# Kernel tuning notes

Measured on AMD Instinct MI355X. Metric: run time of the kernel, lower is better.

## Reference

```python
import jax, jax.numpy as jnp
import numpy as np


def setup_inputs() -> dict:
    key = jax.random.key(0)
    k1, k2, k3, k4 = jax.random.split(key, 4)
    T, B, D, S = 4096, 16, 128, 256
    inputs = jax.random.normal(k1, (T, B, D), dtype=jnp.float32)
    z0 = jnp.zeros((B, S), dtype=jnp.float32)
    # parameters, initialized as in the torch module
    log_neg_a = jnp.full((S,), -0.5, dtype=jnp.float32)
    b = jax.random.normal(k2, (S, D), dtype=jnp.float32) * 0.01
    log_dt = jnp.log(jnp.full((S,), 0.05, dtype=jnp.float32))
    return {"inputs": inputs, "z0": z0, "log_neg_a": log_neg_a, "b": b, "log_dt": log_dt}


def reference(inputs, z0, log_neg_a, b, log_dt):
    # discretized diagonal SSM parameters
    a_real = -jnp.exp(jnp.clip(log_neg_a, -8.0, 4.0))            # [S]
    dt = jnp.exp(jnp.clip(log_dt, -8.0, 1.0))                    # [S]
    a_bar = jnp.exp(dt * a_real)                                 # [S]
    x = dt * a_real
    ratio = jnp.where(jnp.abs(x) < 1e-6, dt, jnp.expm1(x) / a_real)
    b_bar = ratio[:, None] * b                                   # [S, D]

    # precompute input projection for all timesteps: [T, B, S]
    ub = jnp.einsum('tbd,sd->tbs', inputs, b_bar)

    def step(z, u_t):
        z = a_bar[None, :] * z + u_t                             # [B, S]
        return z, z

    _, outs = jax.lax.scan(step, z0, ub)                          # [T, B, S]
    return outs
```

## Files before the change

kernel.cpp:

```cpp
#include <hip/hip_runtime.h>
#include <hip/hip_bf16.h>

#define T_  4096
#define B_  16
#define D_  128
#define S_  256
#define WND 64
#define C4  (T_/WND)

using bf8   = __attribute__((ext_vector_type(8))) short;
using f32x4 = __attribute__((ext_vector_type(4))) float;

__device__ inline float bfbits(unsigned short h) {
    return __builtin_bit_cast(float, (unsigned)h << 16);
}
__device__ inline unsigned short bf16bits(float f) {
    return __hip_bfloat16_raw(__float2bfloat16(f)).x;
}

__global__ __launch_bounds__(256) void k_params(
        const float* __restrict__ lna, const float* __restrict__ bmat,
        const float* __restrict__ ldt,
        float* __restrict__ abar, float* __restrict__ a64,
        __hip_bfloat16* __restrict__ bbar) {
    if (blockIdx.x < 128) {
        int idx = blockIdx.x * 256 + threadIdx.x;
        int s = idx >> 7;
        float la = fminf(fmaxf(lna[s], -8.f), 4.f);
        float ar = -expf(la);
        float lt = fminf(fmaxf(ldt[s], -8.f), 1.f);
        float dt = expf(lt);
        float xx = dt * ar;
        float ratio = (fabsf(xx) < 1e-6f) ? dt : (expm1f(xx) / ar);
        bbar[idx] = __float2bfloat16(ratio * bmat[idx]);
    } else {
        int s = threadIdx.x;
        float la = fminf(fmaxf(lna[s], -8.f), 4.f);
        float ar = -expf(la);
        float lt = fminf(fmaxf(ldt[s], -8.f), 1.f);
        float dt = expf(lt);
        float ab = expf(dt * ar);
        abar[s] = ab;
        float p = ab;
#pragma unroll
        for (int j = 0; j < 6; ++j) p *= p;
        a64[s] = p;
    }
}

__global__ __launch_bounds__(256, 4) void k_gemm(
        const float* __restrict__ x, const __hip_bfloat16* __restrict__ bbar,
        const float* __restrict__ abar,
        __hip_bfloat16* __restrict__ ub, float* __restrict__ e64) {
    const int c = blockIdx.x, b = blockIdx.y;
    __shared__ char LDS[WND * 512];
    const int tid = threadIdx.x, lane = tid & 63, w = tid >> 6;
    const int l15 = lane & 15, l4 = lane >> 4;

    bf8 bfrag[4][4];
#pragma unroll
    for (int j = 0; j < 4; ++j) {
        int s = w * 64 + j * 16 + l15;
#pragma unroll
        for (int kk = 0; kk < 4; ++kk)
            bfrag[j][kk] = *(const bf8*)((const short*)bbar + s * D_ + kk * 32 + l4 * 8);
    }

#pragma unroll
    for (int k = 0; k < 8; ++k) {
        int idx = tid + k * 256;
        int row = idx >> 5, seg = idx & 31;
        float4 v = *(const float4*)(x + ((size_t)(c * WND + row) * B_ + b) * D_ + seg * 4);
        __hip_bfloat162 lo = __float22bfloat162_rn(make_float2(v.x, v.y));
        __hip_bfloat162 hi = __float22bfloat162_rn(make_float2(v.z, v.w));
        uint2 pk = { *(unsigned*)&lo, *(unsigned*)&hi };
        int off = (row * 256 + seg * 8) ^ ((row & 7) << 4);
        *(uint2*)(LDS + off) = pk;
    }
    __syncthreads();

    f32x4 acc[4][4] = {};
#pragma unroll
    for (int i = 0; i < 4; ++i) {
        bf8 af[4];
        int tr = i * 16 + l15;
#pragma unroll
        for (int kk = 0; kk < 4; ++kk) {
            int off = (tr * 256 + kk * 64 + l4 * 16) ^ ((tr & 7) << 4);
            af[kk] = *(const bf8*)(LDS + off);
        }
#pragma unroll
        for (int j = 0; j < 4; ++j)
#pragma unroll
            for (int kk = 0; kk < 4; ++kk)
                acc[i][j] = __builtin_amdgcn_mfma_f32_16x16x32_bf16(
                                af[kk], bfrag[j][kk], acc[i][j], 0, 0, 0);
    }
    __syncthreads();

#pragma unroll
    for (int j = 0; j < 4; ++j) {
        int s = w * 64 + j * 16 + l15;
        float a  = abar[s];
        float a2 = a * a, a4 = a2 * a2, a8 = a4 * a4, a16 = a8 * a8;
        float lf = (l4 == 0) ? a8 * a4 : (l4 == 1) ? a8 : (l4 == 2) ? a4 : 1.f;
        float e = 0.f;
#pragma unroll
        for (int i = 0; i < 4; ++i) {
            unsigned short h0 = bf16bits(acc[i][j][0]);
            unsigned short h1 = bf16bits(acc[i][j][1]);
            unsigned short h2 = bf16bits(acc[i][j][2]);
            unsigned short h3 = bf16bits(acc[i][j][3]);
            float inner = bfbits(h0);
            inner = fmaf(inner, a, bfbits(h1));
            inner = fmaf(inner, a, bfbits(h2));
            inner = fmaf(inner, a, bfbits(h3));
            e = fmaf(e, a16, inner);
            int row0 = i * 16 + l4 * 4;
            *(unsigned short*)(LDS + (((row0    ) * 512 + s * 2) ^ (l4 << 5))) = h0;
            *(unsigned short*)(LDS + (((row0 + 1) * 512 + s * 2) ^ (l4 << 5))) = h1;
            *(unsigned short*)(LDS + (((row0 + 2) * 512 + s * 2) ^ (l4 << 5))) = h2;
            *(unsigned short*)(LDS + (((row0 + 3) * 512 + s * 2) ^ (l4 << 5))) = h3;
        }
        e *= lf;
        e += __shfl_xor(e, 16);
        e += __shfl_xor(e, 32);
        if (l4 == 0) e64[((size_t)c * B_ + b) * S_ + s] = e;
    }
    __syncthreads();

    char* op = (char*)(ub + ((size_t)b * T_ + c * WND) * S_);
#pragma unroll
    for (int k = 0; k < 8; ++k) {
        int o = k * 4096 + tid * 16;
        int swz = (2 * k + (w >> 1)) & 3;
        uint4 v = *(uint4*)(LDS + (o ^ (swz << 5)));
        *(uint4*)(op + o) = v;
    }
}

__global__ __launch_bounds__(256) void k_scan(
        const __hip_bfloat16* __restrict__ ub, const float* __restrict__ e64,
        const float* __restrict__ abar, const float* __restrict__ a64,
        const float* __restrict__ z0, float* __restrict__ out) {
    const int c = blockIdx.x, g = blockIdx.y;
    const int w = threadIdx.x >> 6, lane = threadIdx.x & 63;
    const int b = g * 2 + (w >> 1);
    const int s0 = (w & 1) * 128 + lane * 2;

    float2 a  = *(const float2*)(abar + s0);
    float2 aw = *(const float2*)(a64 + s0);
    float2 z  = *(const float2*)(z0 + b * S_ + s0);

#pragma unroll
    for (int cp0 = 0; cp0 < C4; cp0 += 16) {
        float2 ev[16];
#pragma unroll
        for (int k = 0; k < 16; ++k)
            ev[k] = *(const float2*)(e64 + ((size_t)(cp0 + k) * B_ + b) * S_ + s0);
#pragma unroll
        for (int k = 0; k < 16; ++k) {
            float zx = fmaf(aw.x, z.x, ev[k].x);
            float zy = fmaf(aw.y, z.y, ev[k].y);
            bool p = (cp0 + k) < c;
            z.x = p ? zx : z.x;
            z.y = p ? zy : z.y;
        }
    }

    const char* up = (const char*)(ub + ((size_t)b * T_ + c * WND) * S_ + s0);
    float* op = out + ((size_t)(c * WND) * B_ + b) * S_ + s0;
#pragma unroll 8
    for (int t = 0; t < WND; ++t) {
        ushort2 v = *(const ushort2*)up;
        z.x = fmaf(a.x, z.x, bfbits(v.x));
        z.y = fmaf(a.y, z.y, bfbits(v.y));
        __builtin_nontemporal_store(z.x, op);
        __builtin_nontemporal_store(z.y, op + 1);
        up += S_ * 2;
        op += (size_t)B_ * S_;
    }
}

extern "C" void kernel_launch(void* const* d_in, const int* in_sizes, int n_in,
                              void* d_out, int out_size, void* d_ws, size_t ws_size,
                              hipStream_t stream) {
    const float* x   = (const float*)d_in[0];
    const float* z0  = (const float*)d_in[1];
    const float* lna = (const float*)d_in[2];
    const float* bm  = (const float*)d_in[3];
    const float* ldt = (const float*)d_in[4];
    float* out = (float*)d_out;

    char* ws = (char*)d_ws;
    float*          abar = (float*)ws;
    float*          a64  = (float*)(ws + 4096);
    __hip_bfloat16* bbar = (__hip_bfloat16*)(ws + 8192);
    float*          e64  = (float*)(ws + (128 << 10));
    __hip_bfloat16* ub   = (__hip_bfloat16*)(ws + (4 << 20));

    k_params<<<129, 256, 0, stream>>>(lna, bm, ldt, abar, a64, bbar);
    k_gemm<<<dim3(C4, B_), 256, 0, stream>>>(x, bbar, abar, ub, e64);
    k_scan<<<dim3(C4, B_ / 2), 256, 0, stream>>>(ub, e64, abar, a64, z0, out);
}
```

Before: 48.52 us.

## Process two time chunks per GEMM block with prefetch of the next input tile

Each k_gemm block now handles two consecutive 64-step chunks. It reuses the B fragments loaded into registers and issues the global loads for the second chunk's inputs before computing the first chunk, so load latency overlaps with MFMA work. Shared memory grows to 64KB with separate A and output-staging buffers, and launch bounds drop to 2 blocks per CU. The grid halves to 512 blocks, which reduces parallelism and occupancy and adds register pressure from the prefetched float4 registers.

Result: faster. 45.88 us (-5.5%).

```diff
diff --git a/kernel.cpp b/kernel.cpp
--- a/kernel.cpp
+++ b/kernel.cpp
@@ -48,14 +48,18 @@
     }
 }
 
-__global__ __launch_bounds__(256, 4) void k_gemm(
+__global__ __launch_bounds__(256, 2) void k_gemm(
         const float* __restrict__ x, const __hip_bfloat16* __restrict__ bbar,
         const float* __restrict__ abar,
         __hip_bfloat16* __restrict__ ub, float* __restrict__ e64) {
-    const int c = blockIdx.x, b = blockIdx.y;
-    __shared__ char LDS[WND * 512];
+    const int c0 = blockIdx.x * 2, b = blockIdx.y;
+    __shared__ char LDS[65536];
+    char* A0 = LDS;
+    char* A1 = LDS + 16384;
+    char* P  = LDS + 32768;
     const int tid = threadIdx.x, lane = tid & 63, w = tid >> 6;
     const int l15 = lane & 15, l4 = lane >> 4;
+    const int srow = tid >> 5, sseg = tid & 31;
 
     bf8 bfrag[4][4];
 #pragma unroll
@@ -66,77 +70,107 @@
             bfrag[j][kk] = *(const bf8*)((const short*)bbar + s * D_ + kk * 32 + l4 * 8);
     }
 
-#pragma unroll
-    for (int k = 0; k < 8; ++k) {
-        int idx = tid + k * 256;
-        int row = idx >> 5, seg = idx & 31;
-        float4 v = *(const float4*)(x + ((size_t)(c * WND + row) * B_ + b) * D_ + seg * 4);
-        __hip_bfloat162 lo = __float22bfloat162_rn(make_float2(v.x, v.y));
-        __hip_bfloat162 hi = __float22bfloat162_rn(make_float2(v.z, v.w));
-        uint2 pk = { *(unsigned*)&lo, *(unsigned*)&hi };
-        int off = (row * 256 + seg * 8) ^ ((row & 7) << 4);
-        *(uint2*)(LDS + off) = pk;
-    }
-    __syncthreads();
-
-    f32x4 acc[4][4] = {};
-#pragma unroll
-    for (int i = 0; i < 4; ++i) {
-        bf8 af[4];
-        int tr = i * 16 + l15;
-#pragma unroll
-        for (int kk = 0; kk < 4; ++kk) {
-            int off = (tr * 256 + kk * 64 + l4 * 16) ^ ((tr & 7) << 4);
-            af[kk] = *(const bf8*)(LDS + off);
-        }
-#pragma unroll
-        for (int j = 0; j < 4; ++j)
-#pragma unroll
-            for (int kk = 0; kk < 4; ++kk)
-                acc[i][j] = __builtin_amdgcn_mfma_f32_16x16x32_bf16(
-                                af[kk], bfrag[j][kk], acc[i][j], 0, 0, 0);
-    }
-    __syncthreads();
-
-#pragma unroll
-    for (int j = 0; j < 4; ++j) {
-        int s = w * 64 + j * 16 + l15;
-        float a  = abar[s];
-        float a2 = a * a, a4 = a2 * a2, a8 = a4 * a4, a16 = a8 * a8;
-        float lf = (l4 == 0) ? a8 * a4 : (l4 == 1) ? a8 : (l4 == 2) ? a4 : 1.f;
-        float e = 0.f;
-#pragma unroll
-        for (int i = 0; i < 4; ++i) {
-            unsigned short h0 = bf16bits(acc[i][j][0]);
-            unsigned short h1 = bf16bits(acc[i][j][1]);
-            unsigned short h2 = bf16bits(acc[i][j][2]);
-            unsigned short h3 = bf16bits(acc[i][j][3]);
-            float inner = bfbits(h0);
-            inner = fmaf(inner, a, bfbits(h1));
-            inner = fmaf(inner, a, bfbits(h2));
-            inner = fmaf(inner, a, bfbits(h3));
-            e = fmaf(e, a16, inner);
-            int row0 = i * 16 + l4 * 4;
-            *(unsigned short*)(LDS + (((row0    ) * 512 + s * 2) ^ (l4 << 5))) = h0;
-            *(unsigned short*)(LDS + (((row0 + 1) * 512 + s * 2) ^ (l4 << 5))) = h1;
-            *(unsigned short*)(LDS + (((row0 + 2) * 512 + s * 2) ^ (l4 << 5))) = h2;
-            *(unsigned short*)(LDS + (((row0 + 3) * 512 + s * 2) ^ (l4 << 5))) = h3;
-        }
-        e *= lf;
-        e += __shfl_xor(e, 16);
-        e += __shfl_xor(e, 32);
-        if (l4 == 0) e64[((size_t)c * B_ + b) * S_ + s] = e;
-    }
-    __syncthreads();
-
-    char* op = (char*)(ub + ((size_t)b * T_ + c * WND) * S_);
-#pragma unroll
-    for (int k = 0; k < 8; ++k) {
-        int o = k * 4096 + tid * 16;
-        int swz = (2 * k + (w >> 1)) & 3;
-        uint4 v = *(uint4*)(LDS + (o ^ (swz << 5)));
-        *(uint4*)(op + o) = v;
-    }
+#define LOADX(dst, cc)                                                         \
+    _Pragma("unroll")                                                          \
+    for (int k = 0; k < 8; ++k)                                                \
+        dst[k] = *(const float4*)(x + ((size_t)((cc) * WND + srow + k * 8) * B_ + b) * D_ + sseg * 4);
+
+#define CVTWRITE(A, src)                                                       \
+    _Pragma("unroll")                                                          \
+    for (int k = 0; k < 8; ++k) {                                              \
+        int row = srow + k * 8;                                                \
+        __hip_bfloat162 lo = __float22bfloat162_rn(make_float2(src[k].x, src[k].y)); \
+        __hip_bfloat162 hi = __float22bfloat162_rn(make_float2(src[k].z, src[k].w)); \
+        uint2 pk = { *(unsigned*)&lo, *(unsigned*)&hi };                       \
+        *(uint2*)((A) + ((row * 256 + sseg * 8) ^ ((row & 7) << 4))) = pk;     \
+    }
+
+#define MFMA_TILE(A)                                                           \
+    _Pragma("unroll")                                                          \
+    for (int i = 0; i < 4; ++i) {                                              \
+        bf8 af[4];                                                             \
+        int tr = i * 16 + l15;                                                 \
+        _Pragma("unroll")                                                      \
+        for (int kk = 0; kk < 4; ++kk) {                                       \
+            int off = (tr * 256 + kk * 64 + l4 * 16) ^ ((tr & 7) << 4);        \
+            af[kk] = *(const bf8*)((A) + off);                                 \
+        }                                                                      \
+        _Pragma("unroll")                                                      \
+        for (int j = 0; j < 4; ++j)                                            \
+            _Pragma("unroll")                                                  \
+            for (int kk = 0; kk < 4; ++kk)                                     \
+                acc[i][j] = __builtin_amdgcn_mfma_f32_16x16x32_bf16(           \
+                                af[kk], bfrag[j][kk], acc[i][j], 0, 0, 0);     \
+    }
+
+#define EPILOGUE(cc)                                                           \
+    _Pragma("unroll")                                                          \
+    for (int j = 0; j < 4; ++j) {                                              \
+        int s = w * 64 + j * 16 + l15;                                         \
+        float a  = abar[s];                                                    \
+        float a2 = a * a, a4 = a2 * a2, a8 = a4 * a4, a16 = a8 * a8;           \
+        float lf = (l4 == 0) ? a8 * a4 : (l4 == 1) ? a8 : (l4 == 2) ? a4 : 1.f;\
+        float e = 0.f;                                                         \
+        _Pragma("unroll")                                                      \
+        for (int i = 0; i < 4; ++i) {                                          \
+            unsigned short h0 = bf16bits(acc[i][j][0]);                        \
+            unsigned short h1 = bf16bits(acc[i][j][1]);                        \
+            unsigned short h2 = bf16bits(acc[i][j][2]);                        \
+            unsigned short h3 = bf16bits(acc[i][j][3]);                        \
+            float inner = bfbits(h0);                                          \
+            inner = fmaf(inner, a, bfbits(h1));                                \
+            inner = fmaf(inner, a, bfbits(h2));                                \
+            inner = fmaf(inner, a, bfbits(h3));                                \
+            e = fmaf(e, a16, inner);                                           \
+            int row0 = i * 16 + l4 * 4;                                        \
+            *(unsigned short*)(P + (((row0    ) * 512 + s * 2) ^ (l4 << 5))) = h0; \
+            *(unsigned short*)(P + (((row0 + 1) * 512 + s * 2) ^ (l4 << 5))) = h1; \
+            *(unsigned short*)(P + (((row0 + 2) * 512 + s * 2) ^ (l4 << 5))) = h2; \
+            *(unsigned short*)(P + (((row0 + 3) * 512 + s * 2) ^ (l4 << 5))) = h3; \
+        }                                                                      \
+        e *= lf;                                                               \
+        e += __shfl_xor(e, 16);                                                \
+        e += __shfl_xor(e, 32);                                                \
+        if (l4 == 0) e64[((size_t)(cc) * B_ + b) * S_ + s] = e;                \
+    }
+
+#define FLATCOPY(cc)                                                           \
+    {                                                                          \
+        char* op = (char*)(ub + ((size_t)b * T_ + (cc) * WND) * S_);           \
+        _Pragma("unroll")                                                      \
+        for (int k = 0; k < 8; ++k) {                                          \
+            int o = k * 4096 + tid * 16;                                       \
+            int swz = (2 * k + (w >> 1)) & 3;                                  \
+            uint4 v = *(uint4*)(P + (o ^ (swz << 5)));                         \
+            *(uint4*)(op + o) = v;                                             \
+        }                                                                      \
+    }
+
+    float4 xr[8];
+    LOADX(xr, c0)
+    CVTWRITE(A0, xr)
+    __syncthreads();
+
+    float4 xr1[8];
+    LOADX(xr1, c0 + 1)
+
+    {
+        f32x4 acc[4][4] = {};
+        MFMA_TILE(A0)
+        EPILOGUE(c0)
+    }
+    __syncthreads();
+    FLATCOPY(c0)
+    CVTWRITE(A1, xr1)
+    __syncthreads();
+
+    {
+        f32x4 acc[4][4] = {};
+        MFMA_TILE(A1)
+        EPILOGUE(c0 + 1)
+    }
+    __syncthreads();
+    FLATCOPY(c0 + 1)
 }
 
 __global__ __launch_bounds__(256) void k_scan(
@@ -200,6 +234,6 @@
     __hip_bfloat16* ub   = (__hip_bfloat16*)(ws + (4 << 20));
 
     k_params<<<129, 256, 0, stream>>>(lna, bm, ldt, abar, a64, bbar);
-    k_gemm<<<dim3(C4, B_), 256, 0, stream>>>(x, bbar, abar, ub, e64);
+    k_gemm<<<dim3(C4 / 2, B_), 256, 0, stream>>>(x, bbar, abar, ub, e64);
     k_scan<<<dim3(C4, B_ / 2), 256, 0, stream>>>(ub, e64, abar, a64, z0, out);
 }
```
